# Kernel optimization log

Hardware: AMD Instinct MI355X
Metric: run time of the kernel (lower is better)

The kernel has to match this reference:

```python
import jax, jax.numpy as jnp
import numpy as np

INV_SQRT2 = 0.7071067811865476  # 1/sqrt(2), db1 (Haar) filter coefficient
LEVEL = 3


def _haar_dwt_step(x):
    # x: [B, L] with L even. pywt db1, mode='symmetric', even-length input
    # reduces to exact pairwise: cA[k]=(x[2k]+x[2k+1])/sqrt2, cD[k]=(x[2k]-x[2k+1])/sqrt2
    B, L = x.shape
    p = x.reshape(B, L // 2, 2)
    cA = (p[..., 0] + p[..., 1]) * INV_SQRT2
    cD = (p[..., 0] - p[..., 1]) * INV_SQRT2
    return cA, cD


def setup_inputs() -> dict:
    key = jax.random.key(0)
    x = jax.random.normal(key, (256, 131072), dtype=jnp.float32)
    return {"x": x}


def reference(x) -> jnp.ndarray:
    # pywt.wavedec returns [cA_L, cD_L, cD_{L-1}, ..., cD_1]; the module
    # flattens and concatenates them in that order per sample.
    cA = x
    details = []
    for _ in range(LEVEL):
        cA, cD = _haar_dwt_step(cA)
        details.append(cD)
    return jnp.concatenate([cA] + details[::-1], axis=1)  # [B, L]
```

## Files before the change

kernel.cpp:

```cpp
#include <hip/hip_runtime.h>


#define INV_SQRT2 0.70710678118654752440f

__global__ void __launch_bounds__(256) dwt3_haar_kernel(
    const float* __restrict__ x, float* __restrict__ out) {
    const int L   = 131072;
    const int G   = L >> 3;
    const int gid = blockIdx.x * blockDim.x + threadIdx.x;

    const int row = gid >> 14;
    const int k   = gid & (G - 1);

    const int in_base = row * L + (k << 3);
    const float4 a = *reinterpret_cast<const float4*>(x + in_base);
    const float4 b = *reinterpret_cast<const float4*>(x + in_base + 4);

    const float cA1_0 = (a.x + a.y) * INV_SQRT2;
    const float cD1_0 = (a.x - a.y) * INV_SQRT2;
    const float cA1_1 = (a.z + a.w) * INV_SQRT2;
    const float cD1_1 = (a.z - a.w) * INV_SQRT2;
    const float cA1_2 = (b.x + b.y) * INV_SQRT2;
    const float cD1_2 = (b.x - b.y) * INV_SQRT2;
    const float cA1_3 = (b.z + b.w) * INV_SQRT2;
    const float cD1_3 = (b.z - b.w) * INV_SQRT2;

    const float cA2_0 = (cA1_0 + cA1_1) * INV_SQRT2;
    const float cD2_0 = (cA1_0 - cA1_1) * INV_SQRT2;
    const float cA2_1 = (cA1_2 + cA1_3) * INV_SQRT2;
    const float cD2_1 = (cA1_2 - cA1_3) * INV_SQRT2;

    const float cA3 = (cA2_0 + cA2_1) * INV_SQRT2;
    const float cD3 = (cA2_0 - cA2_1) * INV_SQRT2;

    const int row_out = row * L;
    out[row_out + k]            = cA3;
    out[row_out + (L >> 3) + k] = cD3;

    float2 d2; d2.x = cD2_0; d2.y = cD2_1;
    *reinterpret_cast<float2*>(out + row_out + (L >> 2) + (k << 1)) = d2;

    float4 d1; d1.x = cD1_0; d1.y = cD1_1; d1.z = cD1_2; d1.w = cD1_3;
    *reinterpret_cast<float4*>(out + row_out + (L >> 1) + (k << 2)) = d1;
}

extern "C" void kernel_launch(void* const* d_in, const int* in_sizes, int n_in,
                              void* d_out, int out_size, void* d_ws, size_t ws_size,
                              hipStream_t stream) {
    const float* x = (const float*)d_in[0];
    float* out = (float*)d_out;

    const int total_groups = (256 * 131072) / 8;
    const int block = 256;
    const int grid = total_groups / block;

    dwt3_haar_kernel<<<grid, block, 0, stream>>>(x, out);
}
```

Measured before the change: 47.85 us.

## Process 32 elements per thread with vectorized nontemporal stores

Each thread now handles 32 input samples instead of 8. This lets every output sub-band be written with 16-byte vector stores rather than scalar or float2 stores, and those stores are marked nontemporal so output data does not pollute the cache. The intent is fewer memory instructions and better write efficiency on a bandwidth-bound kernel. The cost is a strided per-instruction load pattern across threads, higher register use per thread, and fewer threads in flight.

```diff
diff --git a/kernel.cpp b/kernel.cpp
--- a/kernel.cpp
+++ b/kernel.cpp
@@ -3,45 +3,73 @@
 
 #define INV_SQRT2 0.70710678118654752440f
 
-__global__ void __launch_bounds__(256) dwt3_haar_kernel(
+typedef float f32x4 __attribute__((ext_vector_type(4)));
+
+__global__ void __launch_bounds__(256) dwt3_haar_kernel32(
     const float* __restrict__ x, float* __restrict__ out) {
     const int L   = 131072;
-    const int G   = L >> 3;
+    const int T   = L >> 5;
     const int gid = blockIdx.x * blockDim.x + threadIdx.x;
 
-    const int row = gid >> 14;
-    const int k   = gid & (G - 1);
+    const int row = gid >> 12;
+    const int t   = gid & (T - 1);
 
-    const int in_base = row * L + (k << 3);
-    const float4 a = *reinterpret_cast<const float4*>(x + in_base);
-    const float4 b = *reinterpret_cast<const float4*>(x + in_base + 4);
+    const int in_base = row * L + (t << 5);
 
-    const float cA1_0 = (a.x + a.y) * INV_SQRT2;
-    const float cD1_0 = (a.x - a.y) * INV_SQRT2;
-    const float cA1_1 = (a.z + a.w) * INV_SQRT2;
-    const float cD1_1 = (a.z - a.w) * INV_SQRT2;
-    const float cA1_2 = (b.x + b.y) * INV_SQRT2;
-    const float cD1_2 = (b.x - b.y) * INV_SQRT2;
-    const float cA1_3 = (b.z + b.w) * INV_SQRT2;
-    const float cD1_3 = (b.z - b.w) * INV_SQRT2;
+    float in[32];
+    #pragma unroll
+    for (int i = 0; i < 8; ++i) {
+        const f32x4 v = *reinterpret_cast<const f32x4*>(x + in_base + 4 * i);
+        in[4 * i + 0] = v.x; in[4 * i + 1] = v.y;
+        in[4 * i + 2] = v.z; in[4 * i + 3] = v.w;
+    }
 
-    const float cA2_0 = (cA1_0 + cA1_1) * INV_SQRT2;
-    const float cD2_0 = (cA1_0 - cA1_1) * INV_SQRT2;
-    const float cA2_1 = (cA1_2 + cA1_3) * INV_SQRT2;
-    const float cD2_1 = (cA1_2 - cA1_3) * INV_SQRT2;
+    float cA1[16], cD1[16];
+    #pragma unroll
+    for (int i = 0; i < 16; ++i) {
+        cA1[i] = (in[2 * i] + in[2 * i + 1]) * INV_SQRT2;
+        cD1[i] = (in[2 * i] - in[2 * i + 1]) * INV_SQRT2;
+    }
 
-    const float cA3 = (cA2_0 + cA2_1) * INV_SQRT2;
-    const float cD3 = (cA2_0 - cA2_1) * INV_SQRT2;
+    float cA2[8], cD2[8];
+    #pragma unroll
+    for (int i = 0; i < 8; ++i) {
+        cA2[i] = (cA1[2 * i] + cA1[2 * i + 1]) * INV_SQRT2;
+        cD2[i] = (cA1[2 * i] - cA1[2 * i + 1]) * INV_SQRT2;
+    }
+
+    float cA3[4], cD3[4];
+    #pragma unroll
+    for (int i = 0; i < 4; ++i) {
+        cA3[i] = (cA2[2 * i] + cA2[2 * i + 1]) * INV_SQRT2;
+        cD3[i] = (cA2[2 * i] - cA2[2 * i + 1]) * INV_SQRT2;
+    }
 
     const int row_out = row * L;
-    out[row_out + k]            = cA3;
-    out[row_out + (L >> 3) + k] = cD3;
 
-    float2 d2; d2.x = cD2_0; d2.y = cD2_1;
-    *reinterpret_cast<float2*>(out + row_out + (L >> 2) + (k << 1)) = d2;
+    f32x4 va3; va3.x = cA3[0]; va3.y = cA3[1]; va3.z = cA3[2]; va3.w = cA3[3];
+    __builtin_nontemporal_store(va3,
+        reinterpret_cast<f32x4*>(out + row_out + (t << 2)));
 
-    float4 d1; d1.x = cD1_0; d1.y = cD1_1; d1.z = cD1_2; d1.w = cD1_3;
-    *reinterpret_cast<float4*>(out + row_out + (L >> 1) + (k << 2)) = d1;
+    f32x4 vd3; vd3.x = cD3[0]; vd3.y = cD3[1]; vd3.z = cD3[2]; vd3.w = cD3[3];
+    __builtin_nontemporal_store(vd3,
+        reinterpret_cast<f32x4*>(out + row_out + (L >> 3) + (t << 2)));
+
+    float* d2p = out + row_out + (L >> 2) + (t << 3);
+    #pragma unroll
+    for (int i = 0; i < 2; ++i) {
+        f32x4 v; v.x = cD2[4 * i]; v.y = cD2[4 * i + 1];
+        v.z = cD2[4 * i + 2]; v.w = cD2[4 * i + 3];
+        __builtin_nontemporal_store(v, reinterpret_cast<f32x4*>(d2p + 4 * i));
+    }
+
+    float* d1p = out + row_out + (L >> 1) + (t << 4);
+    #pragma unroll
+    for (int i = 0; i < 4; ++i) {
+        f32x4 v; v.x = cD1[4 * i]; v.y = cD1[4 * i + 1];
+        v.z = cD1[4 * i + 2]; v.w = cD1[4 * i + 3];
+        __builtin_nontemporal_store(v, reinterpret_cast<f32x4*>(d1p + 4 * i));
+    }
 }
 
 extern "C" void kernel_launch(void* const* d_in, const int* in_sizes, int n_in,
@@ -50,9 +78,9 @@
     const float* x = (const float*)d_in[0];
     float* out = (float*)d_out;
 
-    const int total_groups = (256 * 131072) / 8;
+    const int total_threads = (256 * 131072) / 32;
     const int block = 256;
-    const int grid = total_groups / block;
+    const int grid = total_threads / block;
 
-    dwt3_haar_kernel<<<grid, block, 0, stream>>>(x, out);
+    dwt3_haar_kernel32<<<grid, block, 0, stream>>>(x, out);
 }
```

New measurement: 123.0 us. +157.0%, slower.
